# Kernel optimization log

Hardware: AMD Instinct MI355X
Metric: run time of the kernel (lower is better)

The kernel has to match this reference:

```python
import jax, jax.numpy as jnp
import numpy as np

N_NODES = 100000


def _gcn_layer(x, W, b, src, dst, inv_sqrt_deg):
    # transform first (cheaper when out_dim <= in_dim), then normalized aggregate
    h = x @ W  # [N, out]
    coeff = (inv_sqrt_deg[src] * inv_sqrt_deg[dst])[:, None]  # [E,1] sym norm
    msgs = h[src] * coeff  # [E, out]
    agg = jax.ops.segment_sum(msgs, dst, num_segments=N_NODES)  # [N, out]
    return agg + b


def setup_inputs() -> dict:
    key = jax.random.key(0)
    ks = jax.random.split(key, 8)
    n, e = N_NODES, 1600000
    x = jax.random.normal(ks[0], (n, 256), dtype=jnp.float32)
    src = jax.random.randint(ks[1], (e,), 0, n)
    dst = jax.random.randint(ks[2], (e,), 0, n)
    W1 = jax.random.normal(ks[3], (256, 128), dtype=jnp.float32) * 0.05
    b1 = jax.random.normal(ks[4], (128,), dtype=jnp.float32) * 0.05
    W2 = jax.random.normal(ks[5], (128, 40), dtype=jnp.float32) * 0.05
    b2 = jax.random.normal(ks[6], (40,), dtype=jnp.float32) * 0.05
    return {"x": x, "src": src, "dst": dst, "W1": W1, "b1": b1, "W2": W2, "b2": b2}


def reference(x, src, dst, W1, b1, W2, b2):
    # degree-based symmetric normalization D^{-1/2} A D^{-1/2}
    ones = jnp.ones(src.shape, dtype=x.dtype)
    deg = jax.ops.segment_sum(ones, dst, num_segments=N_NODES)
    inv_sqrt_deg = jnp.where(deg > 0, jax.lax.rsqrt(jnp.maximum(deg, 1.0)), 0.0)
    h = _gcn_layer(x, W1, b1, src, dst, inv_sqrt_deg)
    h = jax.nn.relu(h)
    h = _gcn_layer(h, W2, b2, src, dst, inv_sqrt_deg)
    return h
```

## Files before the change

### kernel.cpp

```cpp
#include <hip/hip_runtime.h>
#include <hip/hip_bf16.h>


#define CHUNK   4096
#define NPB     512
#define NBUCK   196
#define BBCAP   9216

typedef __bf16 bf16x8 __attribute__((ext_vector_type(8)));
typedef float floatx4 __attribute__((ext_vector_type(4)));

__device__ inline unsigned short f2bf(float f) {
    unsigned u = __float_as_uint(f);
    u += 0x7FFF + ((u >> 16) & 1);
    return (unsigned short)(u >> 16);
}
__device__ inline float bflo(unsigned p) { return __uint_as_float(p << 16); }
__device__ inline float bfhi(unsigned p) { return __uint_as_float(p & 0xFFFF0000u); }

__global__ __launch_bounds__(256) void k_f1(const int* __restrict__ src,
                                            const int* __restrict__ dst,
                                            int* __restrict__ gcursor,
                                            unsigned* __restrict__ buckets,
                                            int E, int nchunk,
                                            const float* __restrict__ W1,
                                            unsigned short* __restrict__ w1s,
                                            const float* __restrict__ W2,
                                            unsigned short* __restrict__ w2f,
                                            unsigned* __restrict__ h2z) {
    int t = threadIdx.x;
    if ((int)blockIdx.x >= nchunk + 16) {
        int flat2 = (blockIdx.x - nchunk - 16) * 256 + t;
        int term = flat2 >= 768;
        int u = term ? flat2 - 768 : flat2;
        int kt = u / 192;
        int rm = u - kt * 192;
        int nt = rm >> 6;
        int lane = rm & 63;
        unsigned short vv[8];
        #pragma unroll
        for (int j = 0; j < 8; ++j) {
            int k = kt * 32 + ((lane >> 4) << 3) + j;
            int c = nt * 16 + (lane & 15);
            float wv = (c < 40) ? W2[(size_t)k * 40 + c] : 0.f;
            unsigned short hi = f2bf(wv);
            if (term == 0) vv[j] = hi;
            else vv[j] = f2bf(wv - __uint_as_float((unsigned)hi << 16));
        }
        unsigned short* d = &w2f[(size_t)flat2 * 8];
        *(short4*)(d)     = make_short4(vv[0], vv[1], vv[2], vv[3]);
        *(short4*)(d + 4) = make_short4(vv[4], vv[5], vv[6], vv[7]);
        return;
    }
    if ((int)blockIdx.x >= nchunk) {
        int pb = blockIdx.x - nchunk;
        if (pb == 0 && t < 36) h2z[t] = 0;
        int flat = pb * 256 + t;
        int kt = flat >> 9;
        int nt = (flat >> 6) & 7;
        int lane = flat & 63;
        int kbase = kt * 32 + ((lane >> 4) << 3);
        int n = nt * 16 + (lane & 15);
        unsigned short v[8];
        #pragma unroll
        for (int j = 0; j < 8; ++j) v[j] = f2bf(W1[(size_t)(kbase + j) * 128 + n]);
        unsigned short* d = &w1s[(size_t)flat * 8];
        *(short4*)(d)     = make_short4(v[0], v[1], v[2], v[3]);
        *(short4*)(d + 4) = make_short4(v[4], v[5], v[6], v[7]);
        return;
    }
    __shared__ unsigned srec[CHUNK];
    __shared__ unsigned char sb8[CHUNK];
    __shared__ int hist[NBUCK];
    __shared__ int lbase[NBUCK];
    __shared__ int gbase[NBUCK];
    __shared__ int scanbuf[256];
    int base = blockIdx.x * CHUNK;
    int cnt = min(CHUNK, E - base);
    for (int i = t; i < NBUCK; i += 256) hist[i] = 0;
    __syncthreads();

    unsigned rec[16];
    unsigned br[16];
    bool valid[4];
    #pragma unroll
    for (int k = 0; k < 4; ++k) {
        int e0 = k * 1024 + t * 4;
        valid[k] = (e0 < cnt);
        if (valid[k]) {
            int4 s4 = *(const int4*)&src[base + e0];
            int4 d4 = *(const int4*)&dst[base + e0];
            int ss[4] = {s4.x, s4.y, s4.z, s4.w};
            int dd[4] = {d4.x, d4.y, d4.z, d4.w};
            #pragma unroll
            for (int j = 0; j < 4; ++j) {
                int b = dd[j] >> 9;
                int r = atomicAdd(&hist[b], 1);
                rec[k * 4 + j] = (unsigned)ss[j] | ((unsigned)(dd[j] & 511) << 17);
                br[k * 4 + j] = (unsigned)b | ((unsigned)r << 8);
            }
        }
    }
    __syncthreads();
    scanbuf[t] = (t < NBUCK) ? hist[t] : 0;
    __syncthreads();
    for (int s = 1; s < 256; s <<= 1) {
        int v = (t >= s) ? scanbuf[t - s] : 0;
        __syncthreads();
        scanbuf[t] += v;
        __syncthreads();
    }
    if (t < NBUCK) {
        lbase[t] = scanbuf[t] - hist[t];
        gbase[t] = atomicAdd(&gcursor[t], hist[t]);
    }
    __syncthreads();
    #pragma unroll
    for (int k = 0; k < 4; ++k) {
        if (valid[k]) {
            #pragma unroll
            for (int j = 0; j < 4; ++j) {
                unsigned b = br[k * 4 + j] & 255u;
                unsigned r = br[k * 4 + j] >> 8;
                int p = lbase[b] + (int)r;
                srec[p] = rec[k * 4 + j];
                sb8[p] = (unsigned char)b;
            }
        }
    }
    __syncthreads();
    for (int i = t; i < cnt; i += 256) {
        int b = sb8[i];
        int pos = gbase[b] + (i - lbase[b]);
        if (pos < BBCAP) buckets[(size_t)b * BBCAP + pos] = srec[i];
    }
}

__global__ __launch_bounds__(256) void k_f2(const unsigned* __restrict__ buckets,
                                            const int* __restrict__ gcursor,
                                            int* __restrict__ deg,
                                            int* __restrict__ counter,
                                            int* __restrict__ offsets,
                                            float* __restrict__ isd,
                                            int* __restrict__ csr,
                                            const float* __restrict__ X,
                                            const unsigned short* __restrict__ w1s,
                                            unsigned short* __restrict__ H, int N) {
    __shared__ __align__(16) unsigned char SH[16384];
    int tid = threadIdx.x;
    if ((int)blockIdx.x < NBUCK) {
        int* s_deg = (int*)SH;
        int* s_off = (int*)(SH + 2048);
        int* cur   = (int*)(SH + 4096);
        int* sb    = (int*)(SH + 6144);
        int* sbase = (int*)(SH + 7168);
        int b = blockIdx.x;
        int node0 = b << 9;
        int cnt = min(gcursor[b], BBCAP);
        const unsigned* bk = &buckets[(size_t)b * BBCAP];
        for (int i = tid; i < NPB; i += 256) s_deg[i] = 0;
        __syncthreads();
        for (int i = tid; i < cnt; i += 256)
            atomicAdd(&s_deg[bk[i] >> 17], 1);
        __syncthreads();
        int i0 = tid * 2;
        int na = node0 + i0, nb = node0 + i0 + 1;
        int da = s_deg[i0], db = s_deg[i0 + 1];
        if (na >= N) da = 0;
        if (nb >= N) db = 0;
        int dpa = (da + 15) & ~15, dpb = (db + 15) & ~15;
        sb[tid] = dpa + dpb;
        __syncthreads();
        for (int s = 1; s < 256; s <<= 1) {
            int v = (tid >= s) ? sb[tid - s] : 0;
            __syncthreads();
            sb[tid] += v;
            __syncthreads();
        }
        int excl = sb[tid] - (dpa + dpb);
        if (tid == 0) *sbase = atomicAdd(counter, sb[255]);
        if (b == 0 && tid == 1) isd[N] = 0.f;
        __syncthreads();
        int offa = *sbase + excl;
        int offb = offa + dpa;
        if (na < N) {
            deg[na] = da; offsets[na] = offa;
            isd[na] = (da > 0) ? rsqrtf((float)da) : 0.f;
        }
        if (nb < N) {
            deg[nb] = db; offsets[nb] = offb;
            isd[nb] = (db > 0) ? rsqrtf((float)db) : 0.f;
        }
        s_off[i0] = offa; s_off[i0 + 1] = offb;
        s_deg[i0] = da;   s_deg[i0 + 1] = db;
        cur[i0] = offa;   cur[i0 + 1] = offb;
        __syncthreads();
        for (int i = tid; i < cnt; i += 256) {
            unsigned r = bk[i];
            int p = atomicAdd(&cur[r >> 17], 1);
            csr[p] = (int)(r & 0x1FFFFu);
        }
        __syncthreads();
        for (int i = tid; i < NPB; i += 256) {
            int n = node0 + i;
            if (n < N) {
                int d = s_deg[i];
                int st = s_off[i] + d;
                int en = s_off[i] + ((d + 15) & ~15);
                for (int p = st; p < en; ++p) csr[p] = N;
            }
        }
        return;
    }
    unsigned short* smem = (unsigned short*)SH;
    unsigned short* sA = smem;
    unsigned short* sB = smem + 2048;
    int lane = tid & 63;
    int wave = tid >> 6;
    int wr = wave >> 1;
    int wc = wave & 1;
    int m0 = (blockIdx.x - NBUCK) * 64;

    floatx4 acc[2][4] = {};

    for (int kt = 0; kt < 8; ++kt) {
        #pragma unroll
        for (int i = 0; i < 2; ++i) {
            int f = tid * 2 + i;
            int row = f >> 3;
            int c4 = (f & 7) * 4;
            float4 v = make_float4(0.f, 0.f, 0.f, 0.f);
            int grow = m0 + row;
            if (grow < N) v = *(const float4*)&X[(size_t)grow * 256 + kt * 32 + c4];
            int mt = row >> 4;
            int flane = (row & 15) | ((c4 >> 3) << 4);
            int j0 = c4 & 7;
            unsigned short* d = &sA[(size_t)(mt * 64 + flane) * 8 + j0];
            *(short4*)d = make_short4(f2bf(v.x), f2bf(v.y), f2bf(v.z), f2bf(v.w));
        }
        {
            const float4* srcp = (const float4*)&w1s[(size_t)kt * 4096];
            float4* dstp = (float4*)sB;
            dstp[tid] = srcp[tid];
            dstp[tid + 256] = srcp[tid + 256];
        }
        __syncthreads();
        bf16x8 a[2], b[4];
        #pragma unroll
        for (int p = 0; p < 2; ++p)
            a[p] = *(const bf16x8*)&sA[(size_t)((wr * 2 + p) * 64 + lane) * 8];
        #pragma unroll
        for (int q = 0; q < 4; ++q)
            b[q] = *(const bf16x8*)&sB[(size_t)((wc * 4 + q) * 64 + lane) * 8];
        #pragma unroll
        for (int p = 0; p < 2; ++p)
            #pragma unroll
            for (int q = 0; q < 4; ++q)
                acc[p][q] = __builtin_amdgcn_mfma_f32_16x16x32_bf16(a[p], b[q], acc[p][q], 0, 0, 0);
        __syncthreads();
    }
    #pragma unroll
    for (int p = 0; p < 2; ++p)
        #pragma unroll
        for (int q = 0; q < 4; ++q)
            #pragma unroll
            for (int r = 0; r < 4; ++r) {
                int rl = wr * 32 + p * 16 + ((lane >> 4) << 2) + r;
                int c = wc * 64 + q * 16 + (lane & 15);
                smem[rl * 128 + c] = f2bf(acc[p][q][r]);
            }
    __syncthreads();
    #pragma unroll
    for (int i = 0; i < 4; ++i) {
        int f = tid + i * 256;
        int row = f >> 4;
        int c8 = (f & 15) * 8;
        int grow = m0 + row;
        if (grow <= N)
            *(float4*)&H[(size_t)grow * 128 + c8] = *(const float4*)&smem[row * 128 + c8];
    }
}

__global__ __launch_bounds__(256) void k_agg1(const unsigned* __restrict__ Hu,
                                              const int* __restrict__ csr,
                                              const float* __restrict__ isd,
                                              const int* __restrict__ offsets,
                                              const int* __restrict__ deg,
                                              const float* __restrict__ b1,
                                              unsigned* __restrict__ H1u, int N) {
    int node = __builtin_amdgcn_readfirstlane((blockIdx.x * blockDim.x + threadIdx.x) >> 6);
    int lane = threadIdx.x & 63;
    if (node >= N) return;
    int start = offsets[node];
    int nb = (deg[node] + 15) >> 4;
    float isdn = isd[node];
    float acc0 = 0.f, acc1 = 0.f;
    for (int ib = 0; ib < nb; ++ib) {
        int b0 = start + ib * 16;
        int s[16];
        #pragma unroll
        for (int j = 0; j < 16; ++j) s[j] = csr[b0 + j];
        float iss[16];
        #pragma unroll
        for (int j = 0; j < 16; ++j) iss[j] = isd[s[j]];
        unsigned p[16];
        #pragma unroll
        for (int j = 0; j < 16; ++j) p[j] = Hu[(size_t)s[j] * 64 + lane];
        #pragma unroll
        for (int j = 0; j < 16; ++j) {
            acc0 = fmaf(iss[j], bflo(p[j]), acc0);
            acc1 = fmaf(iss[j], bfhi(p[j]), acc1);
        }
    }
    float r0 = fmaxf(fmaf(isdn, acc0, b1[2 * lane]), 0.f);
    float r1 = fmaxf(fmaf(isdn, acc1, b1[2 * lane + 1]), 0.f);
    H1u[(size_t)node * 64 + lane] = (unsigned)f2bf(r0) | ((unsigned)f2bf(r1) << 16);
}

__global__ __launch_bounds__(256) void k_gemm2(const unsigned short* __restrict__ H1,
                                               const unsigned short* __restrict__ w2f,
                                               const float* __restrict__ isd,
                                               unsigned short* __restrict__ H2s, int N) {
    __shared__ __align__(16) unsigned short sA[8192];
    __shared__ __align__(16) unsigned short sC[64 * 56];
    int tid = threadIdx.x;
    int block_row = blockIdx.x * 64;
    #pragma unroll
    for (int i = 0; i < 4; ++i) {
        int f = tid + i * 256;
        int row = f >> 4;
        int c8 = (f & 15) * 8;
        uint4 v = make_uint4(0, 0, 0, 0);
        int grow = block_row + row;
        if (grow < N) v = *(const uint4*)&H1[(size_t)grow * 128 + c8];
        int kt = c8 >> 5;
        int g  = (c8 >> 3) & 3;
        int mt = row >> 4;
        *(uint4*)&sA[(size_t)((((kt << 2) + mt) << 6) + ((row & 15) | (g << 4))) * 8] = v;
    }
    __syncthreads();
    int wr = tid >> 6;
    int lane = tid & 63;
    floatx4 acc[3] = {};
    #pragma unroll
    for (int kt = 0; kt < 4; ++kt) {
        bf16x8 a = *(const bf16x8*)&sA[(size_t)((((kt << 2) + wr) << 6) + lane) * 8];
        #pragma unroll
        for (int nt = 0; nt < 3; ++nt) {
            bf16x8 bh = *(const bf16x8*)&w2f[(size_t)((kt * 3 + nt) * 64 + lane) * 8];
            bf16x8 bl = *(const bf16x8*)&w2f[(size_t)(768 + (kt * 3 + nt) * 64 + lane) * 8];
            acc[nt] = __builtin_amdgcn_mfma_f32_16x16x32_bf16(a, bh, acc[nt], 0, 0, 0);
            acc[nt] = __builtin_amdgcn_mfma_f32_16x16x32_bf16(a, bl, acc[nt], 0, 0, 0);
        }
    }
    #pragma unroll
    for (int r = 0; r < 4; ++r) {
        int row = wr * 16 + ((lane >> 4) << 2) + r;
        int g = block_row + row;
        float sc = isd[g > N ? N : g];
        #pragma unroll
        for (int nt = 0; nt < 3; ++nt)
            sC[row * 56 + nt * 16 + (lane & 15)] = f2bf(acc[nt][r] * sc);
    }
    __syncthreads();
    if (tid < 64) {
        int grow = block_row + tid;
        if (grow < N) {
            #pragma unroll
            for (int j = 0; j < 5; ++j)
                *(uint4*)&H2s[(size_t)grow * 40 + j * 8] = *(const uint4*)&sC[tid * 56 + j * 8];
        }
    }
}

__global__ __launch_bounds__(256) void k_agg2(const unsigned* __restrict__ Hu2,
                                              const int* __restrict__ csr,
                                              const float* __restrict__ isd,
                                              const int* __restrict__ offsets,
                                              const int* __restrict__ deg,
                                              const float* __restrict__ b2,
                                              float* __restrict__ out, int N) {
    int node = __builtin_amdgcn_readfirstlane((blockIdx.x * blockDim.x + threadIdx.x) >> 6);
    int lane = threadIdx.x & 63;
    if (node >= N) return;
    int start = offsets[node];
    int nb = (deg[node] + 15) >> 4;
    float isdn = isd[node];
    int sub = lane >> 5;
    int c = lane & 31;
    float acc0 = 0.f, acc1 = 0.f;
    for (int ib = 0; ib < nb; ++ib) {
        int b0 = start + ib * 16;
        #pragma unroll
        for (int j = 0; j < 8; ++j) {
            int s = csr[b0 + (j << 1) + sub];
            unsigned q = Hu2[(size_t)s * 20 + c];
            acc0 += bflo(q);
            acc1 += bfhi(q);
        }
    }
    acc0 += __shfl(acc0, lane + 32);
    acc1 += __shfl(acc1, lane + 32);
    if (lane < 20)
        *(float2*)&out[(size_t)node * 40 + 2 * lane] =
            make_float2(fmaf(isdn, acc0, b2[2 * lane]), fmaf(isdn, acc1, b2[2 * lane + 1]));
}

extern "C" void kernel_launch(void* const* d_in, const int* in_sizes, int n_in,
                              void* d_out, int out_size, void* d_ws, size_t ws_size,
                              hipStream_t stream) {
    const float* x  = (const float*)d_in[0];
    const int*  src = (const int*)d_in[1];
    const int*  dst = (const int*)d_in[2];
    const float* W1 = (const float*)d_in[3];
    const float* b1 = (const float*)d_in[4];
    const float* W2 = (const float*)d_in[5];
    const float* b2 = (const float*)d_in[6];
    float* out = (float*)d_out;

    const int N = in_sizes[0] / 256;
    const int E = in_sizes[1];

    char* w = (char*)d_ws;
    auto alloc = [&](size_t bytes) -> void* {
        void* p = (void*)w;
        w += (bytes + 15) & ~(size_t)15;
        return p;
    };
    int*      gcursor = (int*)alloc(256 * 4);
    int*      counter = (int*)alloc(16);
    int*      deg     = (int*)alloc((size_t)N * 4);
    float*    isd     = (float*)alloc((size_t)(N + 1) * 4);
    int*      offsets = (int*)alloc((size_t)(N + 1) * 4);
    unsigned* buckets = (unsigned*)alloc((size_t)NBUCK * BBCAP * 4);
    int*      csr     = (int*)alloc((size_t)(E + 16 * (size_t)N) * 4);
    unsigned short* w1s = (unsigned short*)alloc(32768 * 2);
    unsigned short* w2f = (unsigned short*)alloc(12288 * 2);
    unsigned short* h   = (unsigned short*)alloc((size_t)(N + 1) * 128 * 2);
    unsigned short* h1  = (unsigned short*)alloc((size_t)N * 128 * 2);
    unsigned short* h2  = (unsigned short*)alloc(((size_t)(N + 1) * 20 + 16) * 4);

    hipMemsetAsync(gcursor, 0, 256 * 4 + 16, stream);

    int nchunk = (E + CHUNK - 1) / CHUNK;
    int G1 = (N + 63) / 64;
    k_f1<<<nchunk + 22, 256, 0, stream>>>(src, dst, gcursor, buckets, E, nchunk,
                                          W1, w1s, W2, w2f,
                                          (unsigned*)h2 + (size_t)N * 20);
    k_f2<<<NBUCK + G1, 256, 0, stream>>>(buckets, gcursor, deg, counter, offsets, isd,
                                         csr, x, w1s, h, N);
    k_agg1<<<(N + 3) / 4, 256, 0, stream>>>((const unsigned*)h, csr, isd, offsets, deg,
                                            b1, (unsigned*)h1, N);
    k_gemm2<<<G1, 256, 0, stream>>>(h1, w2f, isd, h2, N);
    k_agg2<<<(N + 3) / 4, 256, 0, stream>>>((const unsigned*)h2, csr, isd, offsets, deg,
                                            b2, out, N);
}
```

Before: 345.2 us.

## Split layer-1 features into column planes and aggregate each plane in separate blocks

The first GEMM now writes its bf16 output into 8 column planes of 16 features each (32 bytes per row per plane), not one 256-byte row per node. The first aggregation launches 8x more blocks, so each block handles one plane. Within a wave, 8 edge slots each gather 8 words of the plane, and partial sums are reduced with cross-lane shuffles. The aim is to shrink the working set per plane so gathers hit cache better, at the cost of reading csr, isd and offsets 8 times and doing extra shuffles.

```diff
diff --git a/kernel.cpp b/kernel.cpp
--- a/kernel.cpp
+++ b/kernel.cpp
@@ -145,7 +145,7 @@
                                             int* __restrict__ csr,
                                             const float* __restrict__ X,
                                             const unsigned short* __restrict__ w1s,
-                                            unsigned short* __restrict__ H, int N) {
+                                            unsigned* __restrict__ Hp, int N) {
     __shared__ __align__(16) unsigned char SH[16384];
     int tid = threadIdx.x;
     if ((int)blockIdx.x < NBUCK) {
@@ -220,6 +220,7 @@
     int wr = wave >> 1;
     int wc = wave & 1;
     int m0 = (blockIdx.x - NBUCK) * 64;
+    size_t HS = (size_t)(N + 1) * 8;
 
     floatx4 acc[2][4] = {};
 
@@ -276,45 +277,63 @@
         int row = f >> 4;
         int c8 = (f & 15) * 8;
         int grow = m0 + row;
-        if (grow <= N)
-            *(float4*)&H[(size_t)grow * 128 + c8] = *(const float4*)&smem[row * 128 + c8];
-    }
-}
-
-__global__ __launch_bounds__(256) void k_agg1(const unsigned* __restrict__ Hu,
+        if (grow <= N) {
+            int cu = c8 >> 1;
+            int plane = cu >> 3;
+            int cin = cu & 7;
+            *(float4*)&Hp[(size_t)plane * HS + (size_t)grow * 8 + cin] =
+                *(const float4*)&smem[row * 128 + c8];
+        }
+    }
+}
+
+__global__ __launch_bounds__(256) void k_agg1(const unsigned* __restrict__ Hp,
                                               const int* __restrict__ csr,
                                               const float* __restrict__ isd,
                                               const int* __restrict__ offsets,
                                               const int* __restrict__ deg,
                                               const float* __restrict__ b1,
                                               unsigned* __restrict__ H1u, int N) {
-    int node = __builtin_amdgcn_readfirstlane((blockIdx.x * blockDim.x + threadIdx.x) >> 6);
+    int p = blockIdx.x & 7;
+    int ng = blockIdx.x >> 3;
+    int wave = threadIdx.x >> 6;
     int lane = threadIdx.x & 63;
+    int node = __builtin_amdgcn_readfirstlane(ng * 4 + wave);
     if (node >= N) return;
     int start = offsets[node];
     int nb = (deg[node] + 15) >> 4;
     float isdn = isd[node];
+    size_t HS = (size_t)(N + 1) * 8;
+    const unsigned* P = Hp + (size_t)p * HS;
+    int e = lane >> 3;
+    int c = lane & 7;
     float acc0 = 0.f, acc1 = 0.f;
     for (int ib = 0; ib < nb; ++ib) {
         int b0 = start + ib * 16;
-        int s[16];
-        #pragma unroll
-        for (int j = 0; j < 16; ++j) s[j] = csr[b0 + j];
-        float iss[16];
-        #pragma unroll
-        for (int j = 0; j < 16; ++j) iss[j] = isd[s[j]];
-        unsigned p[16];
-        #pragma unroll
-        for (int j = 0; j < 16; ++j) p[j] = Hu[(size_t)s[j] * 64 + lane];
-        #pragma unroll
-        for (int j = 0; j < 16; ++j) {
-            acc0 = fmaf(iss[j], bflo(p[j]), acc0);
-            acc1 = fmaf(iss[j], bfhi(p[j]), acc1);
-        }
-    }
-    float r0 = fmaxf(fmaf(isdn, acc0, b1[2 * lane]), 0.f);
-    float r1 = fmaxf(fmaf(isdn, acc1, b1[2 * lane + 1]), 0.f);
-    H1u[(size_t)node * 64 + lane] = (unsigned)f2bf(r0) | ((unsigned)f2bf(r1) << 16);
+        int s0 = csr[b0 + e];
+        int s1 = csr[b0 + 8 + e];
+        float i0 = isd[s0];
+        float i1 = isd[s1];
+        unsigned q0 = P[(size_t)s0 * 8 + c];
+        unsigned q1 = P[(size_t)s1 * 8 + c];
+        acc0 = fmaf(i0, bflo(q0), acc0);
+        acc1 = fmaf(i0, bfhi(q0), acc1);
+        acc0 = fmaf(i1, bflo(q1), acc0);
+        acc1 = fmaf(i1, bfhi(q1), acc1);
+    }
+    acc0 += __shfl_xor(acc0, 8);
+    acc1 += __shfl_xor(acc1, 8);
+    acc0 += __shfl_xor(acc0, 16);
+    acc1 += __shfl_xor(acc1, 16);
+    acc0 += __shfl_xor(acc0, 32);
+    acc1 += __shfl_xor(acc1, 32);
+    if (e == 0) {
+        int col = p * 16 + 2 * c;
+        float r0 = fmaxf(fmaf(isdn, acc0, b1[col]), 0.f);
+        float r1 = fmaxf(fmaf(isdn, acc1, b1[col + 1]), 0.f);
+        H1u[(size_t)node * 64 + p * 8 + c] =
+            (unsigned)f2bf(r0) | ((unsigned)f2bf(r1) << 16);
+    }
 }
 
 __global__ __launch_bounds__(256) void k_gemm2(const unsigned short* __restrict__ H1,
@@ -436,7 +455,7 @@
     int*      csr     = (int*)alloc((size_t)(E + 16 * (size_t)N) * 4);
     unsigned short* w1s = (unsigned short*)alloc(32768 * 2);
     unsigned short* w2f = (unsigned short*)alloc(12288 * 2);
-    unsigned short* h   = (unsigned short*)alloc((size_t)(N + 1) * 128 * 2);
+    unsigned* h = (unsigned*)alloc((size_t)8 * (N + 1) * 8 * 4);
     unsigned short* h1  = (unsigned short*)alloc((size_t)N * 128 * 2);
     unsigned short* h2  = (unsigned short*)alloc(((size_t)(N + 1) * 20 + 16) * 4);
 
@@ -449,8 +468,8 @@
                                           (unsigned*)h2 + (size_t)N * 20);
     k_f2<<<NBUCK + G1, 256, 0, stream>>>(buckets, gcursor, deg, counter, offsets, isd,
                                          csr, x, w1s, h, N);
-    k_agg1<<<(N + 3) / 4, 256, 0, stream>>>((const unsigned*)h, csr, isd, offsets, deg,
-                                            b1, (unsigned*)h1, N);
+    k_agg1<<<(size_t)8 * ((N + 3) / 4), 256, 0, stream>>>(h, csr, isd, offsets, deg,
+                                                          b1, (unsigned*)h1, N);
     k_gemm2<<<G1, 256, 0, stream>>>(h1, w2f, isd, h2, N);
     k_agg2<<<(N + 3) / 4, 256, 0, stream>>>((const unsigned*)h2, csr, isd, offsets, deg,
                                             b2, out, N);
```

New measurement: 507.6 us. 1.47x slower.

## Split layer-2 features into two column halves partitioned across XCDs in agg2

Applied to the files above, without the earlier changes.

The 40-wide bf16 layer-2 feature matrix is stored as two separate 20-column planes (10 words per row). The second aggregation kernel maps blocks so that XCDs 0-3 handle one half and XCDs 4-7 the other, which shrinks each XCD's gathered working set so it fits better in per-XCD L2. Each wave now processes 4 nodes with 16-lane groups over the CSR neighbor list. The cost is more CSR index reads and duplicated offset/degree loads, and some lanes (c>=10) sit idle.

```diff
diff --git a/kernel.cpp b/kernel.cpp
--- a/kernel.cpp
+++ b/kernel.cpp
@@ -27,7 +27,7 @@
                                             unsigned short* __restrict__ w1s,
                                             const float* __restrict__ W2,
                                             unsigned short* __restrict__ w2f,
-                                            unsigned* __restrict__ h2z) {
+                                            unsigned* __restrict__ h2p, int N) {
     int t = threadIdx.x;
     if ((int)blockIdx.x >= nchunk + 16) {
         int flat2 = (blockIdx.x - nchunk - 16) * 256 + t;
@@ -54,7 +54,12 @@
     }
     if ((int)blockIdx.x >= nchunk) {
         int pb = blockIdx.x - nchunk;
-        if (pb == 0 && t < 36) h2z[t] = 0;
+        if (pb == 0 && t < 32) {
+            size_t H2S = (size_t)(N + 1) * 10 + 16;
+            int hh = t >> 4;
+            int i = t & 15;
+            h2p[(size_t)hh * H2S + (size_t)N * 10 + i] = 0;
+        }
         int flat = pb * 256 + t;
         int kt = flat >> 9;
         int nt = (flat >> 6) & 7;
@@ -320,11 +325,12 @@
 __global__ __launch_bounds__(256) void k_gemm2(const unsigned short* __restrict__ H1,
                                                const unsigned short* __restrict__ w2f,
                                                const float* __restrict__ isd,
-                                               unsigned short* __restrict__ H2s, int N) {
+                                               unsigned* __restrict__ H2p, int N) {
     __shared__ __align__(16) unsigned short sA[8192];
     __shared__ __align__(16) unsigned short sC[64 * 56];
     int tid = threadIdx.x;
     int block_row = blockIdx.x * 64;
+    size_t H2S = (size_t)(N + 1) * 10 + 16;
     #pragma unroll
     for (int i = 0; i < 4; ++i) {
         int f = tid + i * 256;
@@ -366,44 +372,95 @@
     if (tid < 64) {
         int grow = block_row + tid;
         if (grow < N) {
+            const unsigned short* s = &sC[tid * 56];
             #pragma unroll
-            for (int j = 0; j < 5; ++j)
-                *(uint4*)&H2s[(size_t)grow * 40 + j * 8] = *(const uint4*)&sC[tid * 56 + j * 8];
-        }
-    }
-}
-
-__global__ __launch_bounds__(256) void k_agg2(const unsigned* __restrict__ Hu2,
+            for (int h = 0; h < 2; ++h) {
+                unsigned* o = &H2p[(size_t)h * H2S + (size_t)grow * 10];
+                #pragma unroll
+                for (int j = 0; j < 5; ++j)
+                    *(uint2*)&o[j * 2] = *(const uint2*)&s[h * 20 + j * 4];
+            }
+        }
+    }
+}
+
+__global__ __launch_bounds__(256) void k_agg2(const unsigned* __restrict__ H2p,
                                               const int* __restrict__ csr,
                                               const float* __restrict__ isd,
                                               const int* __restrict__ offsets,
                                               const int* __restrict__ deg,
                                               const float* __restrict__ b2,
                                               float* __restrict__ out, int N) {
-    int node = __builtin_amdgcn_readfirstlane((blockIdx.x * blockDim.x + threadIdx.x) >> 6);
+    int b = blockIdx.x;
+    int xcd = b & 7;
+    int half = xcd >> 2;
+    int hb = (b >> 3) * 4 + (xcd & 3);
+    int wave = threadIdx.x >> 6;
     int lane = threadIdx.x & 63;
-    if (node >= N) return;
-    int start = offsets[node];
-    int nb = (deg[node] + 15) >> 4;
-    float isdn = isd[node];
-    int sub = lane >> 5;
-    int c = lane & 31;
-    float acc0 = 0.f, acc1 = 0.f;
-    for (int ib = 0; ib < nb; ++ib) {
-        int b0 = start + ib * 16;
-        #pragma unroll
-        for (int j = 0; j < 8; ++j) {
-            int s = csr[b0 + (j << 1) + sub];
-            unsigned q = Hu2[(size_t)s * 20 + c];
-            acc0 += bflo(q);
-            acc1 += bfhi(q);
-        }
-    }
-    acc0 += __shfl(acc0, lane + 32);
-    acc1 += __shfl(acc1, lane + 32);
-    if (lane < 20)
-        *(float2*)&out[(size_t)node * 40 + 2 * lane] =
-            make_float2(fmaf(isdn, acc0, b2[2 * lane]), fmaf(isdn, acc1, b2[2 * lane + 1]));
+    int n0 = __builtin_amdgcn_readfirstlane(hb * 16 + wave * 4);
+    if (n0 >= N) return;
+    size_t H2S = (size_t)(N + 1) * 10 + 16;
+    const unsigned* P = H2p + (size_t)half * H2S;
+    int sub = lane >> 4;
+    int c = lane & 15;
+    int startk[4], nbk[4];
+    float a0[4] = {0.f, 0.f, 0.f, 0.f};
+    float a1[4] = {0.f, 0.f, 0.f, 0.f};
+    int maxnb = 0;
+    #pragma unroll
+    for (int k = 0; k < 4; ++k) {
+        int n = n0 + k;
+        bool v = (n < N);
+        startk[k] = v ? offsets[n] : 0;
+        nbk[k] = v ? (deg[n] + 15) >> 4 : 0;
+        maxnb = max(maxnb, nbk[k]);
+    }
+    for (int ib = 0; ib < maxnb; ++ib) {
+        unsigned q[4][4];
+        #pragma unroll
+        for (int k = 0; k < 4; ++k) {
+            if (ib < nbk[k]) {
+                int b0 = startk[k] + ib * 16;
+                int s[4];
+                #pragma unroll
+                for (int j = 0; j < 4; ++j) s[j] = csr[b0 + (j << 2) + sub];
+                #pragma unroll
+                for (int j = 0; j < 4; ++j)
+                    q[k][j] = (c < 10) ? P[(size_t)s[j] * 10 + c] : 0u;
+            }
+        }
+        #pragma unroll
+        for (int k = 0; k < 4; ++k) {
+            if (ib < nbk[k]) {
+                #pragma unroll
+                for (int j = 0; j < 4; ++j) {
+                    a0[k] += bflo(q[k][j]);
+                    a1[k] += bfhi(q[k][j]);
+                }
+            }
+        }
+    }
+    #pragma unroll
+    for (int k = 0; k < 4; ++k) {
+        a0[k] += __shfl(a0[k], lane + 32);
+        a1[k] += __shfl(a1[k], lane + 32);
+        a0[k] += __shfl(a0[k], lane + 16);
+        a1[k] += __shfl(a1[k], lane + 16);
+    }
+    if (lane < 10) {
+        int col0 = half * 20 + 2 * lane;
+        float bl = b2[col0];
+        float bh = b2[col0 + 1];
+        #pragma unroll
+        for (int k = 0; k < 4; ++k) {
+            int n = n0 + k;
+            if (n < N) {
+                float isdn = isd[n];
+                *(float2*)&out[(size_t)n * 40 + col0] =
+                    make_float2(fmaf(isdn, a0[k], bl), fmaf(isdn, a1[k], bh));
+            }
+        }
+    }
 }
 
 extern "C" void kernel_launch(void* const* d_in, const int* in_sizes, int n_in,
@@ -427,6 +484,7 @@
         w += (bytes + 15) & ~(size_t)15;
         return p;
     };
+    size_t H2S = (size_t)(N + 1) * 10 + 16;
     int*      gcursor = (int*)alloc(256 * 4);
     int*      counter = (int*)alloc(16);
     int*      deg     = (int*)alloc((size_t)N * 4);
@@ -438,20 +496,19 @@
     unsigned short* w2f = (unsigned short*)alloc(12288 * 2);
     unsigned short* h   = (unsigned short*)alloc((size_t)(N + 1) * 128 * 2);
     unsigned short* h1  = (unsigned short*)alloc((size_t)N * 128 * 2);
-    unsigned short* h2  = (unsigned short*)alloc(((size_t)(N + 1) * 20 + 16) * 4);
+    unsigned* h2 = (unsigned*)alloc(2 * H2S * 4);
 
     hipMemsetAsync(gcursor, 0, 256 * 4 + 16, stream);
 
     int nchunk = (E + CHUNK - 1) / CHUNK;
     int G1 = (N + 63) / 64;
     k_f1<<<nchunk + 22, 256, 0, stream>>>(src, dst, gcursor, buckets, E, nchunk,
-                                          W1, w1s, W2, w2f,
-                                          (unsigned*)h2 + (size_t)N * 20);
+                                          W1, w1s, W2, w2f, h2, N);
     k_f2<<<NBUCK + G1, 256, 0, stream>>>(buckets, gcursor, deg, counter, offsets, isd,
                                          csr, x, w1s, h, N);
     k_agg1<<<(N + 3) / 4, 256, 0, stream>>>((const unsigned*)h, csr, isd, offsets, deg,
                                             b1, (unsigned*)h1, N);
     k_gemm2<<<G1, 256, 0, stream>>>(h1, w2f, isd, h2, N);
-    k_agg2<<<(N + 3) / 4, 256, 0, stream>>>((const unsigned*)h2, csr, isd, offsets, deg,
-                                            b2, out, N);
-}
+    int hb2 = (((N + 15) / 16) + 3) & ~3;
+    k_agg2<<<2 * hb2, 256, 0, stream>>>(h2, csr, isd, offsets, deg, b2, out, N);
+}
```

After: 364.2 us. 5.5% more time.

## Fuse layer-1 aggregation with layer-2 GEMM through shared memory

Applied to the files above, without the earlier changes.

Merges the first-layer neighbour aggregation and the second-layer MFMA GEMM into one kernel. Each block aggregates 64 nodes (16 per wave) into an LDS tile, then runs the GEMM on it directly. This removes the H1 intermediate's global write and read and one kernel launch. In exchange, each wave processes 16 nodes serially and far fewer blocks are launched, which cuts parallelism for hiding gather latency. The LDS A-fragment read pattern also changes and could cause bank conflicts.

```diff
diff --git a/kernel.cpp b/kernel.cpp
--- a/kernel.cpp
+++ b/kernel.cpp
@@ -281,82 +281,73 @@
     }
 }
 
-__global__ __launch_bounds__(256) void k_agg1(const unsigned* __restrict__ Hu,
-                                              const int* __restrict__ csr,
-                                              const float* __restrict__ isd,
-                                              const int* __restrict__ offsets,
-                                              const int* __restrict__ deg,
-                                              const float* __restrict__ b1,
-                                              unsigned* __restrict__ H1u, int N) {
-    int node = __builtin_amdgcn_readfirstlane((blockIdx.x * blockDim.x + threadIdx.x) >> 6);
-    int lane = threadIdx.x & 63;
-    if (node >= N) return;
-    int start = offsets[node];
-    int nb = (deg[node] + 15) >> 4;
-    float isdn = isd[node];
-    float acc0 = 0.f, acc1 = 0.f;
-    for (int ib = 0; ib < nb; ++ib) {
-        int b0 = start + ib * 16;
-        int s[16];
-        #pragma unroll
-        for (int j = 0; j < 16; ++j) s[j] = csr[b0 + j];
-        float iss[16];
-        #pragma unroll
-        for (int j = 0; j < 16; ++j) iss[j] = isd[s[j]];
-        unsigned p[16];
-        #pragma unroll
-        for (int j = 0; j < 16; ++j) p[j] = Hu[(size_t)s[j] * 64 + lane];
-        #pragma unroll
-        for (int j = 0; j < 16; ++j) {
-            acc0 = fmaf(iss[j], bflo(p[j]), acc0);
-            acc1 = fmaf(iss[j], bfhi(p[j]), acc1);
-        }
-    }
-    float r0 = fmaxf(fmaf(isdn, acc0, b1[2 * lane]), 0.f);
-    float r1 = fmaxf(fmaf(isdn, acc1, b1[2 * lane + 1]), 0.f);
-    H1u[(size_t)node * 64 + lane] = (unsigned)f2bf(r0) | ((unsigned)f2bf(r1) << 16);
-}
-
-__global__ __launch_bounds__(256) void k_gemm2(const unsigned short* __restrict__ H1,
-                                               const unsigned short* __restrict__ w2f,
-                                               const float* __restrict__ isd,
-                                               unsigned short* __restrict__ H2s, int N) {
-    __shared__ __align__(16) unsigned short sA[8192];
+__global__ __launch_bounds__(256) void k_agg1g2(const unsigned* __restrict__ Hu,
+                                                const int* __restrict__ csr,
+                                                const float* __restrict__ isd,
+                                                const int* __restrict__ offsets,
+                                                const int* __restrict__ deg,
+                                                const float* __restrict__ b1,
+                                                const unsigned short* __restrict__ w2f,
+                                                unsigned short* __restrict__ H2s,
+                                                int N) {
+    __shared__ unsigned sH[64][68];
     __shared__ __align__(16) unsigned short sC[64 * 56];
     int tid = threadIdx.x;
-    int block_row = blockIdx.x * 64;
-    #pragma unroll
-    for (int i = 0; i < 4; ++i) {
-        int f = tid + i * 256;
-        int row = f >> 4;
-        int c8 = (f & 15) * 8;
-        uint4 v = make_uint4(0, 0, 0, 0);
-        int grow = block_row + row;
-        if (grow < N) v = *(const uint4*)&H1[(size_t)grow * 128 + c8];
-        int kt = c8 >> 5;
-        int g  = (c8 >> 3) & 3;
-        int mt = row >> 4;
-        *(uint4*)&sA[(size_t)((((kt << 2) + mt) << 6) + ((row & 15) | (g << 4))) * 8] = v;
-    }
-    __syncthreads();
-    int wr = tid >> 6;
+    int wave = tid >> 6;
     int lane = tid & 63;
+    int base = blockIdx.x * 64;
+    float bl = b1[2 * lane];
+    float bh = b1[2 * lane + 1];
+    for (int i = 0; i < 16; ++i) {
+        int node = __builtin_amdgcn_readfirstlane(base + wave * 16 + i);
+        unsigned outv = 0u;
+        if (node < N) {
+            int start = offsets[node];
+            int nb = (deg[node] + 15) >> 4;
+            float isdn = isd[node];
+            float acc0 = 0.f, acc1 = 0.f;
+            for (int ib = 0; ib < nb; ++ib) {
+                int b0 = start + ib * 16;
+                int s[16];
+                #pragma unroll
+                for (int j = 0; j < 16; ++j) s[j] = csr[b0 + j];
+                float iss[16];
+                #pragma unroll
+                for (int j = 0; j < 16; ++j) iss[j] = isd[s[j]];
+                unsigned p[16];
+                #pragma unroll
+                for (int j = 0; j < 16; ++j) p[j] = Hu[(size_t)s[j] * 64 + lane];
+                #pragma unroll
+                for (int j = 0; j < 16; ++j) {
+                    acc0 = fmaf(iss[j], bflo(p[j]), acc0);
+                    acc1 = fmaf(iss[j], bfhi(p[j]), acc1);
+                }
+            }
+            float r0 = fmaxf(fmaf(isdn, acc0, bl), 0.f);
+            float r1 = fmaxf(fmaf(isdn, acc1, bh), 0.f);
+            outv = (unsigned)f2bf(r0) | ((unsigned)f2bf(r1) << 16);
+        }
+        sH[wave * 16 + i][lane] = outv;
+    }
+    __syncthreads();
+    int wr = wave;
     floatx4 acc[3] = {};
     #pragma unroll
     for (int kt = 0; kt < 4; ++kt) {
-        bf16x8 a = *(const bf16x8*)&sA[(size_t)((((kt << 2) + wr) << 6) + lane) * 8];
+        int arow = wr * 16 + (lane & 15);
+        bf16x8 a = *(const bf16x8*)&sH[arow][kt * 16 + ((lane >> 4) << 2)];
         #pragma unroll
         for (int nt = 0; nt < 3; ++nt) {
-            bf16x8 bh = *(const bf16x8*)&w2f[(size_t)((kt * 3 + nt) * 64 + lane) * 8];
-            bf16x8 bl = *(const bf16x8*)&w2f[(size_t)(768 + (kt * 3 + nt) * 64 + lane) * 8];
-            acc[nt] = __builtin_amdgcn_mfma_f32_16x16x32_bf16(a, bh, acc[nt], 0, 0, 0);
-            acc[nt] = __builtin_amdgcn_mfma_f32_16x16x32_bf16(a, bl, acc[nt], 0, 0, 0);
+            bf16x8 bhf = *(const bf16x8*)&w2f[(size_t)((kt * 3 + nt) * 64 + lane) * 8];
+            bf16x8 blf = *(const bf16x8*)&w2f[(size_t)(768 + (kt * 3 + nt) * 64 + lane) * 8];
+            acc[nt] = __builtin_amdgcn_mfma_f32_16x16x32_bf16(a, bhf, acc[nt], 0, 0, 0);
+            acc[nt] = __builtin_amdgcn_mfma_f32_16x16x32_bf16(a, blf, acc[nt], 0, 0, 0);
         }
     }
     #pragma unroll
     for (int r = 0; r < 4; ++r) {
         int row = wr * 16 + ((lane >> 4) << 2) + r;
-        int g = block_row + row;
+        int g = base + row;
         float sc = isd[g > N ? N : g];
         #pragma unroll
         for (int nt = 0; nt < 3; ++nt)
@@ -364,7 +355,7 @@
     }
     __syncthreads();
     if (tid < 64) {
-        int grow = block_row + tid;
+        int grow = base + tid;
         if (grow < N) {
             #pragma unroll
             for (int j = 0; j < 5; ++j)
@@ -437,7 +428,6 @@
     unsigned short* w1s = (unsigned short*)alloc(32768 * 2);
     unsigned short* w2f = (unsigned short*)alloc(12288 * 2);
     unsigned short* h   = (unsigned short*)alloc((size_t)(N + 1) * 128 * 2);
-    unsigned short* h1  = (unsigned short*)alloc((size_t)N * 128 * 2);
     unsigned short* h2  = (unsigned short*)alloc(((size_t)(N + 1) * 20 + 16) * 4);
 
     hipMemsetAsync(gcursor, 0, 256 * 4 + 16, stream);
@@ -449,9 +439,8 @@
                                           (unsigned*)h2 + (size_t)N * 20);
     k_f2<<<NBUCK + G1, 256, 0, stream>>>(buckets, gcursor, deg, counter, offsets, isd,
                                          csr, x, w1s, h, N);
-    k_agg1<<<(N + 3) / 4, 256, 0, stream>>>((const unsigned*)h, csr, isd, offsets, deg,
-                                            b1, (unsigned*)h1, N);
-    k_gemm2<<<G1, 256, 0, stream>>>(h1, w2f, isd, h2, N);
+    k_agg1g2<<<G1, 256, 0, stream>>>((const unsigned*)h, csr, isd, offsets, deg,
+                                     b1, w2f, h2, N);
     k_agg2<<<(N + 3) / 4, 256, 0, stream>>>((const unsigned*)h2, csr, isd, offsets, deg,
                                             b2, out, N);
 }
```

New measurement: 353.8 us. 2.5% more time.
